# Performance work log

Hardware: AMD Instinct MI355X
Metric: run time of the kernel (lower is better)

## Reference

```python
import jax, jax.numpy as jnp
import numpy as np

N = 50000
E = 800000
D = 128          # feature_dimension
H = 2 * D        # hidden = 2*feature_dimension
C = 8            # num_edge_colours


def setup_inputs() -> dict:
    key = jax.random.key(0)
    ks = jax.random.split(key, 9)
    x = jax.random.normal(ks[0], (N, D), dtype=jnp.float32)
    edge_index = jax.random.randint(ks[1], (2, E), 0, N, dtype=jnp.int64)
    edge_colour = jax.random.randint(ks[2], (E,), 0, C, dtype=jnp.int64)
    # conv weights init: normal(0, 0.001) as in the torch module
    W_conv1 = 0.001 * jax.random.normal(ks[3], (C, H, D), dtype=jnp.float32)
    W_conv2 = 0.001 * jax.random.normal(ks[4], (C, D, H), dtype=jnp.float32)
    # nn.Linear default init: U(-1/sqrt(fan_in), 1/sqrt(fan_in))
    b1 = 1.0 / np.sqrt(D)
    b2 = 1.0 / np.sqrt(H)
    W_self1 = jax.random.uniform(ks[5], (H, D), jnp.float32, -b1, b1)
    b_self1 = jax.random.uniform(ks[6], (H,), jnp.float32, -b1, b1)
    W_self2 = jax.random.uniform(ks[7], (D, H), jnp.float32, -b2, b2)
    b_self2 = jax.random.uniform(ks[8], (D,), jnp.float32, -b2, b2)
    return {
        "x": x, "edge_index": edge_index, "edge_colour": edge_colour,
        "W_self1": W_self1, "b_self1": b_self1,
        "W_self2": W_self2, "b_self2": b_self2,
        "W_conv1": W_conv1, "W_conv2": W_conv2,
    }


def _ec_conv(h, src, seg, Wc):
    # Per-colour gather -> scatter-add -> colour-specific linear, summed over colours.
    # seg = colour * N + dst combines (colour, dst) into one segment id so a single
    # segment_sum covers all colours (equivalent to the per-colour masked loops).
    msgs = h[src]                                             # [E, F]
    agg = jax.ops.segment_sum(msgs, seg, num_segments=C * N)  # [C*N, F]
    agg = agg.reshape(C, N, h.shape[1])                       # [C, N, F]
    return jnp.einsum('cnf,cof->no', agg, Wc)                 # [N, O]


def reference(x, edge_index, edge_colour, W_self1, b_self1, W_self2, b_self2,
              W_conv1, W_conv2):
    src = edge_index[0]   # message() uses x_j = x[src], aggregated at dst
    dst = edge_index[1]
    seg = edge_colour * N + dst
    h = x @ W_self1.T + b_self1 + _ec_conv(x, src, seg, W_conv1)
    h = jax.nn.relu(h)
    h2 = h @ W_self2.T + b_self2 + _ec_conv(h, src, seg, W_conv2)
    return jax.nn.sigmoid(h2 - 10.0)
```

## Files before the change

### kernel.cpp

```cpp
#include <hip/hip_runtime.h>


#define NN 50000
#define EE 800000
#define DD 128
#define HH 256
#define CC 8
#define K1 1152

typedef unsigned short u16;
typedef __attribute__((ext_vector_type(8))) short s16x8;
typedef __attribute__((ext_vector_type(4))) float f32x4;

__device__ __forceinline__ float bf2f(short u) {
  return __uint_as_float(((unsigned)(u16)u) << 16);
}
__device__ __forceinline__ u16 f2bf(float f) {
  unsigned u = __float_as_uint(f);
  u = (u + 0x7FFFu + ((u >> 16) & 1u)) >> 16;
  return (u16)u;
}


__global__ void k_castx(const float* __restrict__ x, u16* __restrict__ xb) {
  int i = blockIdx.x * 256 + threadIdx.x;
  if (i < NN * DD) xb[i] = f2bf(x[i]);
}

__global__ void k_wt1f(const float* __restrict__ Wc1, const float* __restrict__ Ws1,
                       u16* __restrict__ W) {
  int i = blockIdx.x * 256 + threadIdx.x;
  if (i >= 294912) return;
  int e = i & 7;
  int t = i >> 3;
  int rs = t & 15; t >>= 4;
  int kg = t & 3;  t >>= 2;
  int kk = t % 36;
  int col16 = t / 36;
  int col = col16 * 16 + rs;
  int k = kk * 32 + kg * 8 + e;
  float v = (k < CC * DD) ? Wc1[(k >> 7) * (HH * DD) + col * DD + (k & 127)]
                          : Ws1[col * DD + (k - CC * DD)];
  W[i] = f2bf(v);
}

__global__ void k_wt2f(const float* __restrict__ Wc2, const float* __restrict__ Ws2,
                       u16* __restrict__ W) {
  int i = blockIdx.x * 256 + threadIdx.x;
  if (i >= 294912) return;
  int e = i & 7;
  int t = i >> 3;
  int rs = t & 15; t >>= 4;
  int kg = t & 3;  t >>= 2;
  int kk = t & 7;
  int col16 = t >> 3;
  int oc = col16 * 16 + rs;
  int c = oc >> 7, o = oc & 127;
  int k = kk * 32 + kg * 8 + e;
  float v = (c < CC) ? Wc2[c * (DD * HH) + o * HH + k] : Ws2[o * HH + k];
  W[i] = f2bf(v);
}


__global__ void k_hist(const int* __restrict__ ei, const int* __restrict__ ec,
                       int* __restrict__ counts) {
  int e = blockIdx.x * 256 + threadIdx.x;
  if (e < EE) {
    int dst = ei[EE + e];
    int c = ec[e];
    atomicAdd(&counts[dst * CC + c], 1);
  }
}

__global__ void k_offsets(const int* __restrict__ counts, int2* __restrict__ oc,
                          int* __restrict__ cursor, int* __restrict__ gcount) {
  __shared__ int lds[256];
  __shared__ int basesh;
  int tid = threadIdx.x;
  int i = blockIdx.x * 256 + tid;
  int c = (i < CC * NN) ? counts[i] : 0;
  lds[tid] = c;
  __syncthreads();
  int v = c;
  for (int s = 1; s < 256; s <<= 1) {
    int t = (tid >= s) ? lds[tid - s] : 0;
    __syncthreads();
    v += t;
    lds[tid] = v;
    __syncthreads();
  }
  if (tid == 255) basesh = atomicAdd(gcount, v);
  __syncthreads();
  int excl = basesh + v - c;
  if (i < CC * NN) {
    oc[i] = make_int2(excl, c);
    cursor[i] = excl;
  }
}

__global__ void k_fill(const int* __restrict__ ei, const int* __restrict__ ec,
                       int* __restrict__ cursor, int* __restrict__ sv) {
  int e = blockIdx.x * 256 + threadIdx.x;
  if (e < EE) {
    int src = ei[e];
    int dst = ei[EE + e];
    int c = ec[e];
    int slot = atomicAdd(&cursor[dst * CC + c], 1);
    sv[slot] = src * 8 + c;
  }
}


__global__ void __launch_bounds__(256) k_agg1(
    const u16* __restrict__ xb, const int2* __restrict__ oc,
    const int* __restrict__ sv, u16* __restrict__ agg) {
  int item = blockIdx.x * 256 + threadIdx.x;
  int dst = item >> 4, ch = item & 15;
  int eoff = ch * 8;
#pragma unroll
  for (int c = 0; c < CC; ++c) {
    int2 se = oc[dst * CC + c];
    float s[8];
#pragma unroll
    for (int q = 0; q < 8; q++) s[q] = 0.f;
    int j = 0;
    for (; j + 1 < se.y; j += 2) {
      int s0 = sv[se.x + j] >> 3;
      int s1 = sv[se.x + j + 1] >> 3;
      s16x8 v0 = *(const s16x8*)(xb + (size_t)s0 * DD + eoff);
      s16x8 v1 = *(const s16x8*)(xb + (size_t)s1 * DD + eoff);
#pragma unroll
      for (int q = 0; q < 8; q++) s[q] += bf2f(v0[q]) + bf2f(v1[q]);
    }
    if (j < se.y) {
      int s0 = sv[se.x + j] >> 3;
      s16x8 v0 = *(const s16x8*)(xb + (size_t)s0 * DD + eoff);
#pragma unroll
      for (int q = 0; q < 8; q++) s[q] += bf2f(v0[q]);
    }
    s16x8 r;
#pragma unroll
    for (int q = 0; q < 8; q++) r[q] = (short)f2bf(s[q]);
    *(s16x8*)(agg + ((size_t)c * NN + dst) * DD + eoff) = r;
  }
}


__global__ void __launch_bounds__(256, 4) k_gemm1s(
    const u16* __restrict__ xb, const u16* __restrict__ agg,
    const u16* __restrict__ Wf, const float* __restrict__ b1,
    u16* __restrict__ hb) {
  __shared__ u16 Bs[16384];
  int ch = blockIdx.x;
  int rb = blockIdx.y;
  int tid = threadIdx.x;
  int w = tid >> 6, lane = tid & 63;
  int rs = lane & 15, kg = lane >> 4;
  int r0 = rb * 128 + w * 32;

  int rowA[2];
#pragma unroll
  for (int rg = 0; rg < 2; ++rg) rowA[rg] = min(r0 + rg * 16 + rs, NN - 1);

  f32x4 acc[2][8];
#pragma unroll
  for (int rg = 0; rg < 2; ++rg)
#pragma unroll
    for (int i = 0; i < 8; i++)
#pragma unroll
      for (int q = 0; q < 4; q++) acc[rg][i][q] = 0.f;

  for (int ph = 0; ph < 9; ++ph) {
#pragma unroll
    for (int i = 0; i < 8; ++i) {
      int li = i * 256 + tid;
      int fc = li >> 8;
      int u = li & 255;
      int kkl = u >> 6, j = u & 63;
      *(s16x8*)(Bs + (fc * 4 + kkl) * 512 + j * 8) =
          *(const s16x8*)(Wf + (size_t)((ch * 8 + fc) * 36 + ph * 4 + kkl) * 512 + j * 8);
    }
    __syncthreads();

    s16x8 af[2][4];
    if (ph < CC) {
#pragma unroll
      for (int rg = 0; rg < 2; ++rg)
#pragma unroll
        for (int kk = 0; kk < 4; ++kk)
          af[rg][kk] = *(const s16x8*)(agg + ((size_t)ph * NN + rowA[rg]) * DD + kk * 32 + kg * 8);
    } else {
#pragma unroll
      for (int rg = 0; rg < 2; ++rg)
#pragma unroll
        for (int kk = 0; kk < 4; ++kk)
          af[rg][kk] = *(const s16x8*)(xb + (size_t)rowA[rg] * DD + kk * 32 + kg * 8);
    }

#pragma unroll
    for (int kk = 0; kk < 4; ++kk) {
#pragma unroll
      for (int fc = 0; fc < 8; ++fc) {
        s16x8 bfr = *(const s16x8*)(Bs + (fc * 4 + kk) * 512 + lane * 8);
#pragma unroll
        for (int rg = 0; rg < 2; ++rg)
          acc[rg][fc] = __builtin_amdgcn_mfma_f32_16x16x32_bf16(af[rg][kk], bfr, acc[rg][fc], 0, 0, 0);
      }
    }
    __syncthreads();
  }

#pragma unroll
  for (int fc = 0; fc < 8; ++fc) {
    int col = ch * 128 + fc * 16 + rs;
    float bias = b1[col];
#pragma unroll
    for (int rg = 0; rg < 2; ++rg) {
#pragma unroll
      for (int q = 0; q < 4; ++q) {
        float v = acc[rg][fc][q] + bias;
        if (v < 0.f) v = 0.f;
        int rr = r0 + rg * 16 + kg * 4 + q;
        if (rr < NN) hb[(size_t)rr * HH + col] = f2bf(v);
      }
    }
  }
}


__global__ void __launch_bounds__(256, 3) k_gemm2g(
    const u16* __restrict__ hb, const u16* __restrict__ Wf,
    u16* __restrict__ g2) {
  __shared__ u16 Bs[24576];
  int cb = blockIdx.x;
  int rb = blockIdx.y;
  int tid = threadIdx.x;
  int w = tid >> 6, lane = tid & 63;
  int rs = lane & 15, kg = lane >> 4;
  int c16b = cb * 6;

  {
    const u16* src = Wf + (size_t)cb * 24576;
#pragma unroll
    for (int i = 0; i < 12; ++i) {
      int o = (i * 256 + tid) * 8;
      *(s16x8*)(Bs + o) = *(const s16x8*)(src + o);
    }
  }
  __syncthreads();

#pragma unroll
  for (int tt = 0; tt < 2; ++tt) {
    int t = w + tt * 4;
    int r0 = rb * 256 + t * 32;
    int rowA[2];
#pragma unroll
    for (int rg = 0; rg < 2; ++rg) rowA[rg] = min(r0 + rg * 16 + rs, NN - 1);

    s16x8 af[2][8];
#pragma unroll
    for (int rg = 0; rg < 2; ++rg)
#pragma unroll
      for (int kk = 0; kk < 8; ++kk)
        af[rg][kk] = *(const s16x8*)(hb + (size_t)rowA[rg] * HH + kk * 32 + kg * 8);

    f32x4 acc[2][6];
#pragma unroll
    for (int rg = 0; rg < 2; ++rg)
#pragma unroll
      for (int i = 0; i < 6; i++)
#pragma unroll
        for (int q = 0; q < 4; q++) acc[rg][i][q] = 0.f;

#pragma unroll
    for (int kk = 0; kk < 8; ++kk) {
#pragma unroll
      for (int fc = 0; fc < 6; ++fc) {
        s16x8 bfr = *(const s16x8*)(Bs + ((fc * 8 + kk) * 64 + lane) * 8);
#pragma unroll
        for (int rg = 0; rg < 2; ++rg)
          acc[rg][fc] = __builtin_amdgcn_mfma_f32_16x16x32_bf16(af[rg][kk], bfr, acc[rg][fc], 0, 0, 0);
      }
    }

#pragma unroll
    for (int rg = 0; rg < 2; ++rg) {
#pragma unroll
      for (int q = 0; q < 4; ++q) {
        int rr = r0 + rg * 16 + kg * 4 + q;
        if (rr < NN) {
#pragma unroll
          for (int fc = 0; fc < 6; ++fc) {
            int col = (c16b + fc) * 16 + rs;
            g2[(size_t)rr * 1152 + col] = f2bf(acc[rg][fc][q]);
          }
        }
      }
    }
  }
}


__global__ void __launch_bounds__(256) k_final(
    const u16* __restrict__ g2, const float* __restrict__ b2,
    const int2* __restrict__ oc, const int* __restrict__ sv,
    float* __restrict__ out) {
  int item = blockIdx.x * 256 + threadIdx.x;
  if (item >= NN * 8) return;
  int dst = item >> 3, ch = item & 7;
  int eoff = ch * 16;

  int st, cn;
  {
    int2 a0 = oc[dst * CC];
    int2 a7 = oc[dst * CC + 7];
    st = a0.x;
    cn = a7.x + a7.y - a0.x;
  }

  float s[16];
  {
    const u16* sp = g2 + (size_t)dst * 1152 + 1024 + eoff;
    s16x8 lo = *(const s16x8*)sp;
    s16x8 hi = *(const s16x8*)(sp + 8);
#pragma unroll
    for (int q = 0; q < 8; q++) s[q] = b2[eoff + q] + bf2f(lo[q]);
#pragma unroll
    for (int q = 0; q < 8; q++) s[q + 8] = b2[eoff + 8 + q] + bf2f(hi[q]);
  }

  for (int j = 0; j < cn; j += 4) {
    int pofs[4];
#pragma unroll
    for (int t = 0; t < 4; t++) {
      int jj = j + t;
      if (jj < cn) {
        int v = sv[st + jj];
        pofs[t] = (v >> 3) * 1152 + (v & 7) * 128;
      } else {
        pofs[t] = -1;
      }
    }
#pragma unroll
    for (int t = 0; t < 4; t++) {
      if (pofs[t] >= 0) {
        const u16* pp = g2 + pofs[t] + eoff;
        s16x8 lo = *(const s16x8*)pp;
        s16x8 hi = *(const s16x8*)(pp + 8);
#pragma unroll
        for (int q = 0; q < 8; q++) s[q] += bf2f(lo[q]);
#pragma unroll
        for (int q = 0; q < 8; q++) s[q + 8] += bf2f(hi[q]);
      }
    }
  }
  float* op = out + (size_t)dst * DD + eoff;
#pragma unroll
  for (int q = 0; q < 16; q++) op[q] = 1.f / (1.f + expf(10.f - s[q]));
}


extern "C" void kernel_launch(void* const* d_in, const int* in_sizes, int n_in,
                              void* d_out, int out_size, void* d_ws, size_t ws_size,
                              hipStream_t stream) {
  const float* x   = (const float*)d_in[0];
  const int*   ei  = (const int*)d_in[1];
  const int*   ec  = (const int*)d_in[2];
  const float* Ws1 = (const float*)d_in[3];
  const float* b1  = (const float*)d_in[4];
  const float* Ws2 = (const float*)d_in[5];
  const float* b2  = (const float*)d_in[6];
  const float* Wc1 = (const float*)d_in[7];
  const float* Wc2 = (const float*)d_in[8];
  float* out = (float*)d_out;

  char* p = (char*)d_ws;
  u16*  g2     = (u16*)p;
  u16*  agg1   = (u16*)p;
  u16*  xb     = (u16*)(p + 102400000);
  u16*  hb     = (u16*)(p + 115200000);
  u16*  W1f    = (u16*)(p + 140800000);
  u16*  W2f    = (u16*)(p + 141389824);
  int2* oc     = (int2*)(p + 141979648);
  int*  sv     = (int*)(p + 145179648);
  int*  counts = (int*)(p + 148379648);
  int*  gcount = (int*)(p + 149979648);
  int*  cursor = (int*)(p + 149979904);

  hipMemsetAsync(counts, 0, 1600256, stream);

  k_castx<<<25000, 256, 0, stream>>>(x, xb);
  k_wt1f<<<1152, 256, 0, stream>>>(Wc1, Ws1, W1f);
  k_wt2f<<<1152, 256, 0, stream>>>(Wc2, Ws2, W2f);

  k_hist<<<3125, 256, 0, stream>>>(ei, ec, counts);
  k_offsets<<<1563, 256, 0, stream>>>(counts, oc, cursor, gcount);
  k_fill<<<3125, 256, 0, stream>>>(ei, ec, cursor, sv);

  k_agg1<<<3125, 256, 0, stream>>>(xb, oc, sv, agg1);
  k_gemm1s<<<dim3(2, 391), 256, 0, stream>>>(xb, agg1, W1f, b1, hb);
  k_gemm2g<<<dim3(12, 196), 256, 0, stream>>>(hb, W2f, g2);
  k_final<<<1563, 256, 0, stream>>>(g2, b2, oc, sv, out);
}
```

Baseline: 341.0 us.

## Make gemm1 weight-stationary with a full 64-column weight slab in LDS

Restructures the first GEMM so each block loads a 64-column slice of the full K=1152 weight matrix into 144KB of LDS once. It then loops persistently over 784-row chunks, each wave handling 16 rows at a time with all 36 A fragments held in registers. This removes the per-phase weight reload and the extra barriers of the old 9-phase loop. The trade-off is occupancy of one block per CU, heavy register use, and A tiles now read 4 times, once per column block, instead of twice.

```diff
diff --git a/kernel.cpp b/kernel.cpp
--- a/kernel.cpp
+++ b/kernel.cpp
@@ -146,81 +146,63 @@
 }
 
 
-__global__ void __launch_bounds__(256, 4) k_gemm1s(
+__global__ void __launch_bounds__(256, 1) k_gemm1s(
     const u16* __restrict__ xb, const u16* __restrict__ agg,
     const u16* __restrict__ Wf, const float* __restrict__ b1,
     u16* __restrict__ hb) {
-  __shared__ u16 Bs[16384];
-  int ch = blockIdx.x;
+  __shared__ u16 Bs[73728];
+  int cb = blockIdx.x;
   int rb = blockIdx.y;
   int tid = threadIdx.x;
   int w = tid >> 6, lane = tid & 63;
   int rs = lane & 15, kg = lane >> 4;
-  int r0 = rb * 128 + w * 32;
-
-  int rowA[2];
-#pragma unroll
-  for (int rg = 0; rg < 2; ++rg) rowA[rg] = min(r0 + rg * 16 + rs, NN - 1);
-
-  f32x4 acc[2][8];
-#pragma unroll
-  for (int rg = 0; rg < 2; ++rg)
-#pragma unroll
-    for (int i = 0; i < 8; i++)
-#pragma unroll
-      for (int q = 0; q < 4; q++) acc[rg][i][q] = 0.f;
-
-  for (int ph = 0; ph < 9; ++ph) {
-#pragma unroll
-    for (int i = 0; i < 8; ++i) {
-      int li = i * 256 + tid;
-      int fc = li >> 8;
-      int u = li & 255;
-      int kkl = u >> 6, j = u & 63;
-      *(s16x8*)(Bs + (fc * 4 + kkl) * 512 + j * 8) =
-          *(const s16x8*)(Wf + (size_t)((ch * 8 + fc) * 36 + ph * 4 + kkl) * 512 + j * 8);
-    }
-    __syncthreads();
-
-    s16x8 af[2][4];
-    if (ph < CC) {
-#pragma unroll
-      for (int rg = 0; rg < 2; ++rg)
-#pragma unroll
-        for (int kk = 0; kk < 4; ++kk)
-          af[rg][kk] = *(const s16x8*)(agg + ((size_t)ph * NN + rowA[rg]) * DD + kk * 32 + kg * 8);
-    } else {
-#pragma unroll
-      for (int rg = 0; rg < 2; ++rg)
-#pragma unroll
-        for (int kk = 0; kk < 4; ++kk)
-          af[rg][kk] = *(const s16x8*)(xb + (size_t)rowA[rg] * DD + kk * 32 + kg * 8);
-    }
-
-#pragma unroll
-    for (int kk = 0; kk < 4; ++kk) {
-#pragma unroll
-      for (int fc = 0; fc < 8; ++fc) {
-        s16x8 bfr = *(const s16x8*)(Bs + (fc * 4 + kk) * 512 + lane * 8);
-#pragma unroll
-        for (int rg = 0; rg < 2; ++rg)
-          acc[rg][fc] = __builtin_amdgcn_mfma_f32_16x16x32_bf16(af[rg][kk], bfr, acc[rg][fc], 0, 0, 0);
-      }
-    }
-    __syncthreads();
-  }
-
-#pragma unroll
-  for (int fc = 0; fc < 8; ++fc) {
-    int col = ch * 128 + fc * 16 + rs;
-    float bias = b1[col];
-#pragma unroll
-    for (int rg = 0; rg < 2; ++rg) {
+
+  {
+    const u16* src = Wf + (size_t)cb * 73728;
+#pragma unroll
+    for (int i = 0; i < 36; ++i) {
+      int o = (i * 256 + tid) * 8;
+      *(s16x8*)(Bs + o) = *(const s16x8*)(src + o);
+    }
+  }
+  __syncthreads();
+
+  int rend = min(rb * 784 + 784, NN);
+  for (int cst = rb * 784 + w * 16; cst < rend; cst += 64) {
+    int rowA = min(cst + rs, NN - 1);
+    s16x8 af[36];
+#pragma unroll
+    for (int kkg = 0; kkg < 32; ++kkg)
+      af[kkg] = *(const s16x8*)(agg + ((size_t)(kkg >> 2) * NN + rowA) * DD +
+                                (kkg & 3) * 32 + kg * 8);
+#pragma unroll
+    for (int kk = 0; kk < 4; ++kk)
+      af[32 + kk] = *(const s16x8*)(xb + (size_t)rowA * DD + kk * 32 + kg * 8);
+
+    f32x4 acc[4];
+#pragma unroll
+    for (int i = 0; i < 4; i++)
+#pragma unroll
+      for (int q = 0; q < 4; q++) acc[i][q] = 0.f;
+
+#pragma unroll
+    for (int kkg = 0; kkg < 36; ++kkg) {
+#pragma unroll
+      for (int fc = 0; fc < 4; ++fc) {
+        s16x8 bfr = *(const s16x8*)(Bs + (fc * 36 + kkg) * 512 + lane * 8);
+        acc[fc] = __builtin_amdgcn_mfma_f32_16x16x32_bf16(af[kkg], bfr, acc[fc], 0, 0, 0);
+      }
+    }
+
+#pragma unroll
+    for (int fc = 0; fc < 4; ++fc) {
+      int col = cb * 64 + fc * 16 + rs;
+      float bias = b1[col];
 #pragma unroll
       for (int q = 0; q < 4; ++q) {
-        float v = acc[rg][fc][q] + bias;
+        float v = acc[fc][q] + bias;
         if (v < 0.f) v = 0.f;
-        int rr = r0 + rg * 16 + kg * 4 + q;
+        int rr = cst + kg * 4 + q;
         if (rr < NN) hb[(size_t)rr * HH + col] = f2bf(v);
       }
     }
@@ -398,7 +380,7 @@
   k_fill<<<3125, 256, 0, stream>>>(ei, ec, cursor, sv);
 
   k_agg1<<<3125, 256, 0, stream>>>(xb, oc, sv, agg1);
-  k_gemm1s<<<dim3(2, 391), 256, 0, stream>>>(xb, agg1, W1f, b1, hb);
+  k_gemm1s<<<dim3(4, 64), 256, 0, stream>>>(xb, agg1, W1f, b1, hb);
   k_gemm2g<<<dim3(12, 196), 256, 0, stream>>>(hb, W2f, g2);
   k_final<<<1563, 256, 0, stream>>>(g2, b2, oc, sv, out);
 }
```

Result: slower. 504.3 us (+47.9%).

## Double-buffer weight tiles and prefetch A fragments in first GEMM

Applied to the files above, without the earlier changes.

Restructures the k_gemm1s phase loop so the next phase's weight tile is staged into a second LDS buffer and the next A fragments are loaded into alternate registers while MFMAs run on the current ones. This removes one barrier per phase and hides global load latency behind compute. It doubles LDS use to 64 KB and raises register pressure, and launch bounds drop from 4 to 1 block per SM, which can reduce occupancy.

```diff
diff --git a/kernel.cpp b/kernel.cpp
--- a/kernel.cpp
+++ b/kernel.cpp
@@ -146,11 +146,43 @@
 }
 
 
-__global__ void __launch_bounds__(256, 4) k_gemm1s(
+#define LOADA(af, p) do {                                                      \
+  if ((p) < CC) {                                                              \
+    _Pragma("unroll") for (int rg = 0; rg < 2; ++rg)                           \
+    _Pragma("unroll") for (int kk = 0; kk < 4; ++kk)                           \
+      af[rg][kk] = *(const s16x8*)(agg + ((size_t)(p) * NN + rowA[rg]) * DD +  \
+                                   kk * 32 + kg * 8);                          \
+  } else {                                                                     \
+    _Pragma("unroll") for (int rg = 0; rg < 2; ++rg)                           \
+    _Pragma("unroll") for (int kk = 0; kk < 4; ++kk)                           \
+      af[rg][kk] = *(const s16x8*)(xb + (size_t)rowA[rg] * DD +                \
+                                   kk * 32 + kg * 8);                          \
+  } } while (0)
+
+#define STAGE1(p, buf) do {                                                    \
+  _Pragma("unroll") for (int i = 0; i < 8; ++i) {                              \
+    int li = i * 256 + tid;                                                    \
+    int fc = li >> 8; int u = li & 255; int kkl = u >> 6; int j = u & 63;      \
+    *(s16x8*)(Bs + (buf) * 16384 + (fc * 4 + kkl) * 512 + j * 8) =             \
+      *(const s16x8*)(Wf + (size_t)((ch * 8 + fc) * 36 + (p) * 4 + kkl) * 512  \
+                      + j * 8);                                                \
+  } } while (0)
+
+#define MFMAPH(af, buf) do {                                                   \
+  _Pragma("unroll") for (int kk = 0; kk < 4; ++kk)                             \
+  _Pragma("unroll") for (int fc = 0; fc < 8; ++fc) {                           \
+    s16x8 bfr = *(const s16x8*)(Bs + (buf) * 16384 + (fc * 4 + kk) * 512 +     \
+                                lane * 8);                                     \
+    _Pragma("unroll") for (int rg = 0; rg < 2; ++rg)                           \
+      acc[rg][fc] = __builtin_amdgcn_mfma_f32_16x16x32_bf16(af[rg][kk], bfr,   \
+                                                            acc[rg][fc], 0, 0, 0); \
+  } } while (0)
+
+__global__ void __launch_bounds__(256, 1) k_gemm1s(
     const u16* __restrict__ xb, const u16* __restrict__ agg,
     const u16* __restrict__ Wf, const float* __restrict__ b1,
     u16* __restrict__ hb) {
-  __shared__ u16 Bs[16384];
+  __shared__ u16 Bs[32768];
   int ch = blockIdx.x;
   int rb = blockIdx.y;
   int tid = threadIdx.x;
@@ -170,43 +202,19 @@
 #pragma unroll
       for (int q = 0; q < 4; q++) acc[rg][i][q] = 0.f;
 
+  s16x8 afA[2][4], afB[2][4];
+  STAGE1(0, 0);
+  LOADA(afA, 0);
+  __syncthreads();
+
+#pragma unroll
   for (int ph = 0; ph < 9; ++ph) {
-#pragma unroll
-    for (int i = 0; i < 8; ++i) {
-      int li = i * 256 + tid;
-      int fc = li >> 8;
-      int u = li & 255;
-      int kkl = u >> 6, j = u & 63;
-      *(s16x8*)(Bs + (fc * 4 + kkl) * 512 + j * 8) =
-          *(const s16x8*)(Wf + (size_t)((ch * 8 + fc) * 36 + ph * 4 + kkl) * 512 + j * 8);
-    }
-    __syncthreads();
-
-    s16x8 af[2][4];
-    if (ph < CC) {
-#pragma unroll
-      for (int rg = 0; rg < 2; ++rg)
-#pragma unroll
-        for (int kk = 0; kk < 4; ++kk)
-          af[rg][kk] = *(const s16x8*)(agg + ((size_t)ph * NN + rowA[rg]) * DD + kk * 32 + kg * 8);
-    } else {
-#pragma unroll
-      for (int rg = 0; rg < 2; ++rg)
-#pragma unroll
-        for (int kk = 0; kk < 4; ++kk)
-          af[rg][kk] = *(const s16x8*)(xb + (size_t)rowA[rg] * DD + kk * 32 + kg * 8);
-    }
-
-#pragma unroll
-    for (int kk = 0; kk < 4; ++kk) {
-#pragma unroll
-      for (int fc = 0; fc < 8; ++fc) {
-        s16x8 bfr = *(const s16x8*)(Bs + (fc * 4 + kk) * 512 + lane * 8);
-#pragma unroll
-        for (int rg = 0; rg < 2; ++rg)
-          acc[rg][fc] = __builtin_amdgcn_mfma_f32_16x16x32_bf16(af[rg][kk], bfr, acc[rg][fc], 0, 0, 0);
-      }
-    }
+    const int pb = ph & 1;
+    if (ph < 8) {
+      STAGE1(ph + 1, pb ^ 1);
+      if (pb == 0) { LOADA(afB, ph + 1); } else { LOADA(afA, ph + 1); }
+    }
+    if (pb == 0) { MFMAPH(afA, 0); } else { MFMAPH(afB, 1); }
     __syncthreads();
   }
 
```

Measured after the change: 344.4 us. No clear change (+1.0%).
